# Optimization experiments

Measured on AMD Instinct MI355X. Metric: run time of the kernel, lower is better.

## Reference

```python
import jax, jax.numpy as jnp
import numpy as np

SEQ, IN_DIM, OUT_DIM = 8192, 1024, 1024

def setup_inputs() -> dict:
    key = jax.random.key(0)
    k1, k2, k3, k4 = jax.random.split(key, 4)
    inputs = jax.random.normal(k1, (SEQ, IN_DIM), dtype=jnp.float32)
    # torch.nn.Linear stores weight as [out_dim, in_dim]; y = x @ W.T
    w_query = jax.random.normal(k2, (OUT_DIM, IN_DIM), dtype=jnp.float32) * (1.0 / np.sqrt(IN_DIM))
    w_key = jax.random.normal(k3, (OUT_DIM, IN_DIM), dtype=jnp.float32) * (1.0 / np.sqrt(IN_DIM))
    w_value = jax.random.normal(k4, (OUT_DIM, IN_DIM), dtype=jnp.float32) * (1.0 / np.sqrt(IN_DIM))
    return {"inputs": inputs, "w_query": w_query, "w_key": w_key, "w_value": w_value}

def reference(inputs, w_query, w_key, w_value):
    # QKV projections: [S, D_out]
    q = inputs @ w_query.T
    k = inputs @ w_key.T
    v = inputs @ w_value.T
    scale = 1.0 / jnp.sqrt(jnp.asarray(k.shape[-1], dtype=q.dtype))
    scores = (q @ k.T) * scale  # [S, S]
    # causal mask: lower-triangular kept, upper set to -inf
    s = scores.shape[0]
    causal = jnp.tril(jnp.ones((s, s), dtype=bool))
    scores = jnp.where(causal, scores, -jnp.inf)
    attn = jax.nn.softmax(scores, axis=-1)
    return attn @ v
```

## Files before the change

### kernel.cpp

```cpp
#include <hip/hip_runtime.h>
#include <stdint.h>
#include <stddef.h>


#define SEQ   8192
#define DIM   1024

typedef __bf16 bf16x8 __attribute__((ext_vector_type(8)));
typedef float  f32x4  __attribute__((ext_vector_type(4)));

#define MFMA16(a, b, c) __builtin_amdgcn_mfma_f32_16x16x32_bf16((a), (b), (c), 0, 0, 0)

__device__ __forceinline__ uint16_t f2bf(float f) {
  uint32_t u = __builtin_bit_cast(uint32_t, f);
  return (uint16_t)((u + 0x7fffu + ((u >> 16) & 1u)) >> 16);
}
__device__ __forceinline__ float bf2f(uint16_t h) {
  uint32_t u = ((uint32_t)h) << 16;
  return __builtin_bit_cast(float, u);
}

typedef const __attribute__((address_space(1))) uint32_t* gas_t;
typedef __attribute__((address_space(3))) uint32_t* las_t;
__device__ __forceinline__ void async16(const void* g, void* l) {
  __builtin_amdgcn_global_load_lds((gas_t)g, (las_t)l, 16, 0, 0);
}

__global__ __launch_bounds__(256) void cast_all(const float* __restrict__ x,
                                                const float* __restrict__ wq,
                                                const float* __restrict__ wk,
                                                const float* __restrict__ wv,
                                                uint16_t* __restrict__ xb,
                                                uint16_t* __restrict__ wcat) {
  int b = blockIdx.x;
  const float* src;
  uint16_t* dst;
  int i;
  if (b < 8192) {
    src = x; dst = xb; i = (b * 256 + threadIdx.x) * 4;
  } else {
    int wb = b - 8192;
    int sel = wb >> 10;
    src = sel == 0 ? wq : (sel == 1 ? wk : wv);
    dst = wcat + sel * 1048576;
    i = ((wb & 1023) * 256 + threadIdx.x) * 4;
  }
  float4 v = *(const float4*)(src + i);
  ushort4 o;
  o.x = f2bf(v.x); o.y = f2bf(v.y); o.z = f2bf(v.z); o.w = f2bf(v.w);
  *(ushort4*)(dst + i) = o;
}

__global__ __launch_bounds__(256) void qkv_gemm(const uint16_t* __restrict__ A,
                                                const uint16_t* __restrict__ B,
                                                uint16_t* __restrict__ Qblk,
                                                uint16_t* __restrict__ Kblk,
                                                uint16_t* __restrict__ Vblk) {
  __shared__ __align__(16) uint16_t As[128 * 64];
  __shared__ __align__(16) uint16_t Bs[128 * 64];
  const int t    = threadIdx.x;
  const int w    = t >> 6;
  const int lane = t & 63;
  const int lm   = lane & 15;
  const int qd   = lane >> 4;
  const int wrow = (w >> 1) * 64;
  const int wcol = (w & 1) * 64;
  const int rowbase = blockIdx.y * 128;
  const int colbase = blockIdx.x * 128;

  const int lrow = lane >> 3;
  const int lgrp = (lane & 7) ^ (lrow & 7);

  f32x4 acc[4][4] = {};

  for (int kb = 0; kb < DIM; kb += 64) {
    __syncthreads();
#pragma unroll
    for (int rep = 0; rep < 4; ++rep) {
      int r0 = rep * 32 + w * 8;
      async16(A + (size_t)(rowbase + r0 + lrow) * DIM + kb + lgrp * 8, As + r0 * 64);
      async16(B + (size_t)(colbase + r0 + lrow) * DIM + kb + lgrp * 8, Bs + r0 * 64);
    }
    __syncthreads();
#pragma unroll
    for (int kc = 0; kc < 2; ++kc) {
      bf16x8 af[4], bfr[4];
#pragma unroll
      for (int mt = 0; mt < 4; ++mt) {
        int r = wrow + mt * 16 + lm;
        af[mt] = *(const bf16x8*)(As + r * 64 + (((kc * 4 + qd) ^ (lm & 7)) * 8));
      }
#pragma unroll
      for (int nt = 0; nt < 4; ++nt) {
        int r = wcol + nt * 16 + lm;
        bfr[nt] = *(const bf16x8*)(Bs + r * 64 + (((kc * 4 + qd) ^ (lm & 7)) * 8));
      }
#pragma unroll
      for (int mt = 0; mt < 4; ++mt)
#pragma unroll
        for (int nt = 0; nt < 4; ++nt)
          acc[mt][nt] = MFMA16(af[mt], bfr[nt], acc[mt][nt]);
    }
  }

#pragma unroll
  for (int mt = 0; mt < 4; ++mt)
#pragma unroll
    for (int nt = 0; nt < 4; ++nt)
#pragma unroll
      for (int r = 0; r < 4; ++r) {
        int m = rowbase + wrow + mt * 16 + qd * 4 + r;
        int n = colbase + wcol + nt * 16 + lm;
        uint16_t v = f2bf(acc[mt][nt][r]);
        int nn = n & 1023;
        if (n < 2048) {
          size_t off = (((size_t)(m >> 4) * 32 + (nn >> 5)) * 64 +
                        ((nn >> 3) & 3) * 16 + (m & 15)) * 8 + (nn & 7);
          if (n < 1024) Qblk[off] = v; else Kblk[off] = v;
        } else {
          size_t off = (((size_t)(nn >> 4) * 256 + (m >> 5)) * 64 +
                        ((m >> 3) & 3) * 16 + (nn & 15)) * 8 + (m & 7);
          Vblk[off] = v;
        }
      }
}

__global__ __launch_bounds__(512, 2) void attn_kernel(const uint16_t* __restrict__ Qblk,
                                                      const uint16_t* __restrict__ Kblk,
                                                      const uint16_t* __restrict__ Vblk,
                                                      uint16_t* __restrict__ P0,
                                                      uint16_t* __restrict__ P1,
                                                      float* __restrict__ Mm,
                                                      float* __restrict__ Ll) {
  __shared__ __align__(16) uint16_t Qs[32768];
  __shared__ __align__(16) uint16_t Pb[8192];
  __shared__ float stats[32][8];
  __shared__ float mrow[32];

  const int t    = threadIdx.x;
  const int w    = t >> 6;
  const int lane = t & 63;
  const int lm   = lane & 15;
  const int qd   = lane >> 4;
  const int par  = blockIdx.x & 1;
  const int p    = blockIdx.x >> 1;
  const float c1 = 0.045084220027780106f;

#pragma unroll 1
  for (int half = 0; half < 2; ++half) {
    const int tt   = half ? 255 - p : p;
    const int row0 = tt * 32;
    const int jn   = (tt >> 3) + 1;

    __syncthreads();
#pragma unroll
    for (int i = 0; i < 8; ++i)
      async16(Qblk + ((size_t)(tt * 64 + w * 8 + i)) * 512 + lane * 8,
              Qs + (w * 8 + i) * 512);

    bf16x8 kpre0[4], kpre1[4];
    {
      const uint16_t* kbp0 = Kblk + ((size_t)(par * 16 + w * 2) * 32) * 512 + lane * 8;
#pragma unroll
      for (int c = 0; c < 4; ++c) {
        kpre0[c] = *(const bf16x8*)(kbp0 + (size_t)c * 512);
        kpre1[c] = *(const bf16x8*)(kbp0 + (size_t)(32 + c) * 512);
      }
    }
    __syncthreads();

    float m_run[2][4], l_run[2][4];
#pragma unroll
    for (int mt = 0; mt < 2; ++mt)
#pragma unroll
      for (int r = 0; r < 4; ++r) { m_run[mt][r] = -1e30f; l_run[mt][r] = 0.0f; }
    f32x4 o_acc[2][8] = {};

#pragma unroll 1
    for (int jg = par; jg < jn; jg += 2) {
      const uint16_t* kbp = Kblk + ((size_t)(jg * 16 + w * 2) * 32) * 512 + lane * 8;
      const uint16_t* vbp = Vblk + ((size_t)(w * 8) * 256 + jg * 8) * 512 + lane * 8;
      const uint16_t* qsp = Qs + lane * 8;

      f32x4 sacc[2][2] = {};
      bf16x8 kr0[8], kr1[8];
#pragma unroll
      for (int c = 0; c < 4; ++c) { kr0[c] = kpre0[c]; kr1[c] = kpre1[c]; }
#pragma unroll
      for (int c = 4; c < 8; ++c) {
        kr0[c] = *(const bf16x8*)(kbp + (size_t)c * 512);
        kr1[c] = *(const bf16x8*)(kbp + (size_t)(32 + c) * 512);
      }
#pragma unroll
      for (int kb = 0; kb < 32; ++kb) {
        bf16x8 q0 = *(const bf16x8*)(qsp + kb * 512);
        bf16x8 q1 = *(const bf16x8*)(qsp + (32 + kb) * 512);
        sacc[0][0] = MFMA16(q0, kr0[kb & 7], sacc[0][0]);
        sacc[1][0] = MFMA16(q1, kr0[kb & 7], sacc[1][0]);
        sacc[0][1] = MFMA16(q0, kr1[kb & 7], sacc[0][1]);
        sacc[1][1] = MFMA16(q1, kr1[kb & 7], sacc[1][1]);
        if (kb < 24) {
          kr0[kb & 7] = *(const bf16x8*)(kbp + (size_t)(kb + 8) * 512);
          kr1[kb & 7] = *(const bf16x8*)(kbp + (size_t)(32 + kb + 8) * 512);
        }
      }

      if (jg == jn - 1) {
#pragma unroll
        for (int mt = 0; mt < 2; ++mt)
#pragma unroll
          for (int nt = 0; nt < 2; ++nt)
#pragma unroll
            for (int r = 0; r < 4; ++r) {
              int col = jg * 256 + w * 32 + nt * 16 + lm;
              int row = row0 + mt * 16 + qd * 4 + r;
              if (col > row) sacc[mt][nt][r] = -1e30f;
            }
      }

#pragma unroll
      for (int mt = 0; mt < 2; ++mt)
#pragma unroll
        for (int r = 0; r < 4; ++r) {
          float v = fmaxf(sacc[mt][0][r], sacc[mt][1][r]);
          v = fmaxf(v, __shfl_xor(v, 1));
          v = fmaxf(v, __shfl_xor(v, 2));
          v = fmaxf(v, __shfl_xor(v, 4));
          v = fmaxf(v, __shfl_xor(v, 8));
          if (lm == 0) stats[mt * 16 + qd * 4 + r][w] = v;
        }
      __syncthreads();

      bf16x8 vr0[8], vr1[8];
#pragma unroll
      for (int dt = 0; dt < 8; ++dt) {
        vr0[dt] = *(const bf16x8*)(vbp + ((size_t)dt * 256 + 0) * 512);
        vr1[dt] = *(const bf16x8*)(vbp + ((size_t)dt * 256 + 1) * 512);
      }

      float alpha[2][4], psum[2][4];
#pragma unroll
      for (int mt = 0; mt < 2; ++mt)
#pragma unroll
        for (int r = 0; r < 4; ++r) {
          int rl = mt * 16 + qd * 4 + r;
          float4 g0 = *(const float4*)&stats[rl][0];
          float4 g1 = *(const float4*)&stats[rl][4];
          float gm = fmaxf(fmaxf(fmaxf(g0.x, g0.y), fmaxf(g0.z, g0.w)),
                           fmaxf(fmaxf(g1.x, g1.y), fmaxf(g1.z, g1.w)));
          float mn = fmaxf(m_run[mt][r], gm);
          alpha[mt][r] = exp2f((m_run[mt][r] - mn) * c1);
          m_run[mt][r] = mn;
          psum[mt][r] = 0.0f;
        }
#pragma unroll
      for (int mt = 0; mt < 2; ++mt)
#pragma unroll
        for (int nt = 0; nt < 2; ++nt)
#pragma unroll
          for (int r = 0; r < 4; ++r) {
            float pv = exp2f((sacc[mt][nt][r] - m_run[mt][r]) * c1);
            psum[mt][r] += pv;
            Pb[((mt * 8 + w) * 64 + (nt * 2 + (lm >> 3)) * 16 + qd * 4 + r) * 8 +
               (lm & 7)] = f2bf(pv);
          }
#pragma unroll
      for (int mt = 0; mt < 2; ++mt)
#pragma unroll
        for (int r = 0; r < 4; ++r) {
          float s2 = psum[mt][r];
          s2 += __shfl_xor(s2, 1);
          s2 += __shfl_xor(s2, 2);
          s2 += __shfl_xor(s2, 4);
          s2 += __shfl_xor(s2, 8);
          l_run[mt][r] = l_run[mt][r] * alpha[mt][r] + s2;
        }
      __syncthreads();

      {
        const uint16_t* kbpn = Kblk + ((size_t)((jg + 2) * 16 + w * 2) * 32) * 512 + lane * 8;
#pragma unroll
        for (int c = 0; c < 4; ++c) {
          kpre0[c] = *(const bf16x8*)(kbpn + (size_t)c * 512);
          kpre1[c] = *(const bf16x8*)(kbpn + (size_t)(32 + c) * 512);
        }
      }

#pragma unroll
      for (int mt = 0; mt < 2; ++mt)
#pragma unroll
        for (int dt = 0; dt < 8; ++dt)
#pragma unroll
          for (int r = 0; r < 4; ++r)
            o_acc[mt][dt][r] *= alpha[mt][r];

#pragma unroll
      for (int kc = 0; kc < 8; ++kc) {
        bf16x8 pf0 = *(const bf16x8*)(Pb + (kc * 64 + lane) * 8);
        bf16x8 pf1 = *(const bf16x8*)(Pb + ((8 + kc) * 64 + lane) * 8);
#pragma unroll
        for (int dt = 0; dt < 8; ++dt) {
          bf16x8 vf = (kc & 1) ? vr1[dt] : vr0[dt];
          o_acc[0][dt] = MFMA16(pf0, vf, o_acc[0][dt]);
          o_acc[1][dt] = MFMA16(pf1, vf, o_acc[1][dt]);
        }
        if (kc < 6) {
#pragma unroll
          for (int dt = 0; dt < 8; ++dt) {
            if (kc & 1)
              vr1[dt] = *(const bf16x8*)(vbp + ((size_t)dt * 256 + kc + 2) * 512);
            else
              vr0[dt] = *(const bf16x8*)(vbp + ((size_t)dt * 256 + kc + 2) * 512);
          }
        }
      }
    }

    if (lm == 0) {
#pragma unroll
      for (int mt = 0; mt < 2; ++mt)
#pragma unroll
        for (int r = 0; r < 4; ++r) {
          int rl = mt * 16 + qd * 4 + r;
          stats[rl][w] = l_run[mt][r];
          if (w == 0) mrow[rl] = m_run[mt][r];
        }
    }
    __syncthreads();
    if (t < 32) {
      float4 a0 = *(const float4*)&stats[t][0];
      float4 a1 = *(const float4*)&stats[t][4];
      Mm[par * SEQ + row0 + t] = mrow[t];
      Ll[par * SEQ + row0 + t] = (a0.x + a0.y + a0.z + a0.w) + (a1.x + a1.y + a1.z + a1.w);
    }
    uint16_t* Pp = par ? P1 : P0;
#pragma unroll
    for (int mt = 0; mt < 2; ++mt)
#pragma unroll
      for (int dt = 0; dt < 8; ++dt)
#pragma unroll
        for (int r = 0; r < 4; ++r) {
          int row = row0 + mt * 16 + qd * 4 + r;
          int d   = w * 128 + dt * 16 + lm;
          Pp[(size_t)row * DIM + d] = f2bf(o_acc[mt][dt][r]);
        }
  }
}

__global__ __launch_bounds__(256) void merge_kernel(const uint16_t* __restrict__ P0,
                                                    const uint16_t* __restrict__ P1,
                                                    const float* __restrict__ Mm,
                                                    const float* __restrict__ Ll,
                                                    float* __restrict__ out) {
  const int row = blockIdx.x;
  const int d0  = threadIdx.x * 4;
  const float c1 = 0.045084220027780106f;
  float m0 = Mm[row], m1 = Mm[SEQ + row];
  float l0 = Ll[row], l1 = Ll[SEQ + row];
  float m  = fmaxf(m0, m1);
  float a0 = exp2f((m0 - m) * c1);
  float a1 = exp2f((m1 - m) * c1);
  float inv = 1.0f / (a0 * l0 + a1 * l1);
  ushort4 p0 = *(const ushort4*)(P0 + (size_t)row * DIM + d0);
  ushort4 p1 = *(const ushort4*)(P1 + (size_t)row * DIM + d0);
  float4 o;
  o.x = (a0 * bf2f(p0.x) + a1 * bf2f(p1.x)) * inv;
  o.y = (a0 * bf2f(p0.y) + a1 * bf2f(p1.y)) * inv;
  o.z = (a0 * bf2f(p0.z) + a1 * bf2f(p1.z)) * inv;
  o.w = (a0 * bf2f(p0.w) + a1 * bf2f(p1.w)) * inv;
  *(float4*)(out + (size_t)row * DIM + d0) = o;
}

extern "C" void kernel_launch(void* const* d_in, const int* in_sizes, int n_in,
                              void* d_out, int out_size, void* d_ws, size_t ws_size,
                              hipStream_t stream) {
  (void)in_sizes; (void)n_in; (void)out_size; (void)ws_size;
  const float* x  = (const float*)d_in[0];
  const float* wq = (const float*)d_in[1];
  const float* wk = (const float*)d_in[2];
  const float* wv = (const float*)d_in[3];
  float* out = (float*)d_out;

  char* ws = (char*)d_ws;
  uint16_t* Qblk = (uint16_t*)(ws);
  uint16_t* Kblk = (uint16_t*)(ws + 16777216);
  uint16_t* Vblk = (uint16_t*)(ws + 33554432);
  uint16_t* P0   = (uint16_t*)(ws + 50331648);
  uint16_t* xb   = (uint16_t*)(ws + 67108864);
  uint16_t* P1   = (uint16_t*)(ws + 67108864);
  uint16_t* wcat = (uint16_t*)(ws + 83886080);
  float*    Mm   = (float*)(ws + 83886080);
  float*    Ll   = (float*)(ws + 83886080 + 65536);

  cast_all<<<11264, 256, 0, stream>>>(x, wq, wk, wv, xb, wcat);
  qkv_gemm<<<dim3(24, 64), 256, 0, stream>>>(xb, wcat, Qblk, Kblk, Vblk);
  attn_kernel<<<256, 512, 0, stream>>>(Qblk, Kblk, Vblk, P0, P1, Mm, Ll);
  merge_kernel<<<SEQ, 256, 0, stream>>>(P0, P1, Mm, Ll, out);
}
```

Baseline: 535.2 us.

## Double query tile to 64 rows per block and split P staging across wave halves

The attention kernel now processes 64 query rows per block instead of 32, doubling the Q tile in shared memory and the per-wave accumulators so that each K and V fragment loaded from global memory feeds four MFMA row tiles instead of two. The P tile is staged through the same shared buffer in two phases, with waves 0-3 writing first and waves 4-7 second, which adds extra barriers. The explicit K/V register prefetch pipelining is removed in favour of direct loads. The intent is to halve K/V global traffic per query row, at the cost of far more registers and shared memory, likely lowering occupancy and risking spills under the 2-blocks launch bound.

```diff
diff --git a/kernel.cpp b/kernel.cpp
--- a/kernel.cpp
+++ b/kernel.cpp
@@ -132,82 +132,63 @@
                                                       uint16_t* __restrict__ P1,
                                                       float* __restrict__ Mm,
                                                       float* __restrict__ Ll) {
-  __shared__ __align__(16) uint16_t Qs[32768];
+  __shared__ __align__(16) uint16_t Qs[65536];
   __shared__ __align__(16) uint16_t Pb[8192];
-  __shared__ float stats[32][8];
-  __shared__ float mrow[32];
+  __shared__ float stats[64][8];
+  __shared__ float mrow[64];
 
   const int t    = threadIdx.x;
   const int w    = t >> 6;
   const int lane = t & 63;
   const int lm   = lane & 15;
   const int qd   = lane >> 4;
+  const int wk   = w & 3;
+  const int wp   = w >> 2;
   const int par  = blockIdx.x & 1;
   const int p    = blockIdx.x >> 1;
   const float c1 = 0.045084220027780106f;
 
 #pragma unroll 1
   for (int half = 0; half < 2; ++half) {
-    const int tt   = half ? 255 - p : p;
-    const int row0 = tt * 32;
-    const int jn   = (tt >> 3) + 1;
-
-    __syncthreads();
-#pragma unroll
-    for (int i = 0; i < 8; ++i)
-      async16(Qblk + ((size_t)(tt * 64 + w * 8 + i)) * 512 + lane * 8,
-              Qs + (w * 8 + i) * 512);
-
-    bf16x8 kpre0[4], kpre1[4];
-    {
-      const uint16_t* kbp0 = Kblk + ((size_t)(par * 16 + w * 2) * 32) * 512 + lane * 8;
-#pragma unroll
-      for (int c = 0; c < 4; ++c) {
-        kpre0[c] = *(const bf16x8*)(kbp0 + (size_t)c * 512);
-        kpre1[c] = *(const bf16x8*)(kbp0 + (size_t)(32 + c) * 512);
-      }
-    }
-    __syncthreads();
-
-    float m_run[2][4], l_run[2][4];
-#pragma unroll
-    for (int mt = 0; mt < 2; ++mt)
+    const int tt   = half ? 127 - p : p;
+    const int row0 = tt * 64;
+    const int jn   = (tt >> 2) + 1;
+
+    __syncthreads();
+#pragma unroll
+    for (int i = 0; i < 16; ++i)
+      async16(Qblk + (size_t)tt * 65536 + i * 4096 + w * 512 + lane * 8,
+              Qs + i * 4096 + w * 512);
+    __syncthreads();
+
+    float m_run[4][4], l_run[4][4];
+#pragma unroll
+    for (int mt = 0; mt < 4; ++mt)
 #pragma unroll
       for (int r = 0; r < 4; ++r) { m_run[mt][r] = -1e30f; l_run[mt][r] = 0.0f; }
-    f32x4 o_acc[2][8] = {};
+    f32x4 o_acc[4][8] = {};
 
 #pragma unroll 1
     for (int jg = par; jg < jn; jg += 2) {
       const uint16_t* kbp = Kblk + ((size_t)(jg * 16 + w * 2) * 32) * 512 + lane * 8;
-      const uint16_t* vbp = Vblk + ((size_t)(w * 8) * 256 + jg * 8) * 512 + lane * 8;
       const uint16_t* qsp = Qs + lane * 8;
 
-      f32x4 sacc[2][2] = {};
-      bf16x8 kr0[8], kr1[8];
-#pragma unroll
-      for (int c = 0; c < 4; ++c) { kr0[c] = kpre0[c]; kr1[c] = kpre1[c]; }
-#pragma unroll
-      for (int c = 4; c < 8; ++c) {
-        kr0[c] = *(const bf16x8*)(kbp + (size_t)c * 512);
-        kr1[c] = *(const bf16x8*)(kbp + (size_t)(32 + c) * 512);
-      }
-#pragma unroll
+      f32x4 sacc[4][2] = {};
+#pragma unroll 4
       for (int kb = 0; kb < 32; ++kb) {
-        bf16x8 q0 = *(const bf16x8*)(qsp + kb * 512);
-        bf16x8 q1 = *(const bf16x8*)(qsp + (32 + kb) * 512);
-        sacc[0][0] = MFMA16(q0, kr0[kb & 7], sacc[0][0]);
-        sacc[1][0] = MFMA16(q1, kr0[kb & 7], sacc[1][0]);
-        sacc[0][1] = MFMA16(q0, kr1[kb & 7], sacc[0][1]);
-        sacc[1][1] = MFMA16(q1, kr1[kb & 7], sacc[1][1]);
-        if (kb < 24) {
-          kr0[kb & 7] = *(const bf16x8*)(kbp + (size_t)(kb + 8) * 512);
-          kr1[kb & 7] = *(const bf16x8*)(kbp + (size_t)(32 + kb + 8) * 512);
+        bf16x8 k0 = *(const bf16x8*)(kbp + (size_t)kb * 512);
+        bf16x8 k1 = *(const bf16x8*)(kbp + (size_t)(16384 + kb * 512));
+#pragma unroll
+        for (int mt = 0; mt < 4; ++mt) {
+          bf16x8 q = *(const bf16x8*)(qsp + (mt * 32 + kb) * 512);
+          sacc[mt][0] = MFMA16(q, k0, sacc[mt][0]);
+          sacc[mt][1] = MFMA16(q, k1, sacc[mt][1]);
         }
       }
 
       if (jg == jn - 1) {
 #pragma unroll
-        for (int mt = 0; mt < 2; ++mt)
+        for (int mt = 0; mt < 4; ++mt)
 #pragma unroll
           for (int nt = 0; nt < 2; ++nt)
 #pragma unroll
@@ -219,7 +200,7 @@
       }
 
 #pragma unroll
-      for (int mt = 0; mt < 2; ++mt)
+      for (int mt = 0; mt < 4; ++mt)
 #pragma unroll
         for (int r = 0; r < 4; ++r) {
           float v = fmaxf(sacc[mt][0][r], sacc[mt][1][r]);
@@ -231,16 +212,11 @@
         }
       __syncthreads();
 
-      bf16x8 vr0[8], vr1[8];
-#pragma unroll
-      for (int dt = 0; dt < 8; ++dt) {
-        vr0[dt] = *(const bf16x8*)(vbp + ((size_t)dt * 256 + 0) * 512);
-        vr1[dt] = *(const bf16x8*)(vbp + ((size_t)dt * 256 + 1) * 512);
-      }
-
-      float alpha[2][4], psum[2][4];
-#pragma unroll
-      for (int mt = 0; mt < 2; ++mt)
+      float alpha[4][4];
+      uint32_t pvp[4][2][2];
+#pragma unroll
+      for (int mt = 0; mt < 4; ++mt) {
+        float psum[4];
 #pragma unroll
         for (int r = 0; r < 4; ++r) {
           int rl = mt * 16 + qd * 4 + r;
@@ -251,74 +227,102 @@
           float mn = fmaxf(m_run[mt][r], gm);
           alpha[mt][r] = exp2f((m_run[mt][r] - mn) * c1);
           m_run[mt][r] = mn;
-          psum[mt][r] = 0.0f;
-        }
-#pragma unroll
-      for (int mt = 0; mt < 2; ++mt)
+          psum[r] = 0.0f;
+        }
 #pragma unroll
         for (int nt = 0; nt < 2; ++nt)
 #pragma unroll
-          for (int r = 0; r < 4; ++r) {
-            float pv = exp2f((sacc[mt][nt][r] - m_run[mt][r]) * c1);
-            psum[mt][r] += pv;
-            Pb[((mt * 8 + w) * 64 + (nt * 2 + (lm >> 3)) * 16 + qd * 4 + r) * 8 +
-               (lm & 7)] = f2bf(pv);
+          for (int rp = 0; rp < 2; ++rp) {
+            float pv0 = exp2f((sacc[mt][nt][rp * 2 + 0] - m_run[mt][rp * 2 + 0]) * c1);
+            float pv1 = exp2f((sacc[mt][nt][rp * 2 + 1] - m_run[mt][rp * 2 + 1]) * c1);
+            psum[rp * 2 + 0] += pv0;
+            psum[rp * 2 + 1] += pv1;
+            pvp[mt][nt][rp] = (uint32_t)f2bf(pv0) | ((uint32_t)f2bf(pv1) << 16);
           }
 #pragma unroll
-      for (int mt = 0; mt < 2; ++mt)
-#pragma unroll
         for (int r = 0; r < 4; ++r) {
-          float s2 = psum[mt][r];
+          float s2 = psum[r];
           s2 += __shfl_xor(s2, 1);
           s2 += __shfl_xor(s2, 2);
           s2 += __shfl_xor(s2, 4);
           s2 += __shfl_xor(s2, 8);
           l_run[mt][r] = l_run[mt][r] * alpha[mt][r] + s2;
         }
+      }
+      if (wp == 0) {
+#pragma unroll
+        for (int mt = 0; mt < 4; ++mt)
+#pragma unroll
+          for (int nt = 0; nt < 2; ++nt)
+#pragma unroll
+            for (int rp = 0; rp < 2; ++rp) {
+              int base = ((mt * 4 + wk) * 64 + (nt * 2 + (lm >> 3)) * 16 + qd * 4 + rp * 2) * 8 +
+                         (lm & 7);
+              Pb[base]     = (uint16_t)(pvp[mt][nt][rp] & 0xffff);
+              Pb[base + 8] = (uint16_t)(pvp[mt][nt][rp] >> 16);
+            }
+      }
       __syncthreads();
 
-      {
-        const uint16_t* kbpn = Kblk + ((size_t)((jg + 2) * 16 + w * 2) * 32) * 512 + lane * 8;
-#pragma unroll
-        for (int c = 0; c < 4; ++c) {
-          kpre0[c] = *(const bf16x8*)(kbpn + (size_t)c * 512);
-          kpre1[c] = *(const bf16x8*)(kbpn + (size_t)(32 + c) * 512);
-        }
-      }
-
-#pragma unroll
-      for (int mt = 0; mt < 2; ++mt)
+#pragma unroll
+      for (int mt = 0; mt < 4; ++mt)
 #pragma unroll
         for (int dt = 0; dt < 8; ++dt)
 #pragma unroll
           for (int r = 0; r < 4; ++r)
             o_acc[mt][dt][r] *= alpha[mt][r];
 
-#pragma unroll
-      for (int kc = 0; kc < 8; ++kc) {
-        bf16x8 pf0 = *(const bf16x8*)(Pb + (kc * 64 + lane) * 8);
-        bf16x8 pf1 = *(const bf16x8*)(Pb + ((8 + kc) * 64 + lane) * 8);
+      const uint16_t* vbp = Vblk + (((size_t)(w * 8) * 256 + jg * 8) * 64) * 8 + lane * 8;
+#pragma unroll
+      for (int kc = 0; kc < 4; ++kc) {
+        bf16x8 pf[4];
+#pragma unroll
+        for (int mt = 0; mt < 4; ++mt)
+          pf[mt] = *(const bf16x8*)(Pb + ((mt * 4 + kc) * 64 + lane) * 8);
 #pragma unroll
         for (int dt = 0; dt < 8; ++dt) {
-          bf16x8 vf = (kc & 1) ? vr1[dt] : vr0[dt];
-          o_acc[0][dt] = MFMA16(pf0, vf, o_acc[0][dt]);
-          o_acc[1][dt] = MFMA16(pf1, vf, o_acc[1][dt]);
-        }
-        if (kc < 6) {
-#pragma unroll
-          for (int dt = 0; dt < 8; ++dt) {
-            if (kc & 1)
-              vr1[dt] = *(const bf16x8*)(vbp + ((size_t)dt * 256 + kc + 2) * 512);
-            else
-              vr0[dt] = *(const bf16x8*)(vbp + ((size_t)dt * 256 + kc + 2) * 512);
-          }
+          bf16x8 vf = *(const bf16x8*)(vbp + ((size_t)dt * 256 + kc) * 512);
+#pragma unroll
+          for (int mt = 0; mt < 4; ++mt)
+            o_acc[mt][dt] = MFMA16(pf[mt], vf, o_acc[mt][dt]);
+        }
+      }
+      __syncthreads();
+      if (wp == 1) {
+#pragma unroll
+        for (int mt = 0; mt < 4; ++mt)
+#pragma unroll
+          for (int nt = 0; nt < 2; ++nt)
+#pragma unroll
+            for (int rp = 0; rp < 2; ++rp) {
+              int base = ((mt * 4 + wk) * 64 + (nt * 2 + (lm >> 3)) * 16 + qd * 4 + rp * 2) * 8 +
+                         (lm & 7);
+              Pb[base]     = (uint16_t)(pvp[mt][nt][rp] & 0xffff);
+              Pb[base + 8] = (uint16_t)(pvp[mt][nt][rp] >> 16);
+            }
+      }
+      __syncthreads();
+
+#pragma unroll
+      for (int kc = 0; kc < 4; ++kc) {
+        bf16x8 pf[4];
+#pragma unroll
+        for (int mt = 0; mt < 4; ++mt)
+          pf[mt] = *(const bf16x8*)(Pb + ((mt * 4 + kc) * 64 + lane) * 8);
+#pragma unroll
+        for (int dt = 0; dt < 8; ++dt) {
+          bf16x8 vf = *(const bf16x8*)(vbp + ((size_t)dt * 256 + 4 + kc) * 512);
+#pragma unroll
+          for (int mt = 0; mt < 4; ++mt)
+            o_acc[mt][dt] = MFMA16(pf[mt], vf, o_acc[mt][dt]);
         }
       }
     }
 
+    __syncthreads();
     if (lm == 0) {
 #pragma unroll
-      for (int mt = 0; mt < 2; ++mt)
+      for (int mt = 0; mt < 4; ++mt)
 #pragma unroll
         for (int r = 0; r < 4; ++r) {
           int rl = mt * 16 + qd * 4 + r;
@@ -327,7 +331,7 @@
         }
     }
     __syncthreads();
-    if (t < 32) {
+    if (t < 64) {
       float4 a0 = *(const float4*)&stats[t][0];
       float4 a1 = *(const float4*)&stats[t][4];
       Mm[par * SEQ + row0 + t] = mrow[t];
@@ -335,7 +339,7 @@
     }
     uint16_t* Pp = par ? P1 : P0;
 #pragma unroll
-    for (int mt = 0; mt < 2; ++mt)
+    for (int mt = 0; mt < 4; ++mt)
 #pragma unroll
       for (int dt = 0; dt < 8; ++dt)
 #pragma unroll
```

Result: slower. 1.189 ms (+122.1%).
